# Performance work log

Measured on AMD Instinct MI355X. Metric: run time of the kernel, lower is better.

The kernel has to match this reference:

```python
import jax, jax.numpy as jnp
import numpy as np

EPS = 1e-5


def hyper_graph_conv(x, elements, W, b):
    """x: [B, C, N] vertex features; elements: [M, 8] vertex ids per hex element.
    Gather 8 vertex features per element, apply Linear(8C -> 8Co) on the
    concatenated features, then scatter-mean the 8 outputs back to vertices.
    Returns [B, Co, N]."""
    B, C, N = x.shape
    M = elements.shape[0]
    Co = W.shape[0] // 8
    g = x[:, :, elements]                      # [B, C, M, 8]
    g = jnp.transpose(g, (0, 2, 3, 1)).reshape(B, M, 8 * C)   # [B, M, 8C]
    h = jnp.einsum('bmk,ok->bmo', g, W) + b    # [B, M, 8Co]
    h = h.reshape(B, M * 8, Co)                # per-(element,corner) vertex outputs
    flat = elements.reshape(-1)                # [M*8]
    out = jnp.zeros((B, N, Co), dtype=x.dtype).at[:, flat, :].add(h)
    cnt = jnp.zeros((N,), dtype=x.dtype).at[flat].add(1.0)
    out = out / jnp.maximum(cnt, 1.0)[None, :, None]
    return jnp.transpose(out, (0, 2, 1))       # [B, Co, N]


def batch_norm(x, gamma, beta):
    # BatchNorm1d in training mode over [B, C, N]: stats over (B, N)
    mean = jnp.mean(x, axis=(0, 2), keepdims=True)
    var = jnp.mean(jnp.square(x - mean), axis=(0, 2), keepdims=True)
    xn = (x - mean) * jax.lax.rsqrt(var + EPS)
    return xn * gamma[None, :, None] + beta[None, :, None]


def setup_inputs() -> dict:
    key = jax.random.key(0)
    ks = jax.random.split(key, 8)
    B, Cin, Cout, N, M = 4, 8, 16, 100000, 98304
    return {
        'x': jax.random.normal(ks[0], (B, Cin, N), dtype=jnp.float32),
        'elements': jax.random.randint(ks[1], (M, 8), 0, N, dtype=jnp.int32),
        'W1': jax.random.normal(ks[2], (8 * Cout, 8 * Cin), dtype=jnp.float32) * (1.0 / np.sqrt(8 * Cin)),
        'b1': jnp.zeros((8 * Cout,), dtype=jnp.float32),
        'gamma1': jnp.ones((Cout,), dtype=jnp.float32),
        'beta1': jnp.zeros((Cout,), dtype=jnp.float32),
        'W2': jax.random.normal(ks[3], (8 * Cout, 8 * Cout), dtype=jnp.float32) * (1.0 / np.sqrt(8 * Cout)),
        'b2': jnp.zeros((8 * Cout,), dtype=jnp.float32),
        'gamma2': jnp.ones((Cout,), dtype=jnp.float32),
        'beta2': jnp.zeros((Cout,), dtype=jnp.float32),
        'Wskip': jax.random.normal(ks[4], (Cout, Cin), dtype=jnp.float32) * (1.0 / np.sqrt(Cin)),
        'bskip': jnp.zeros((Cout,), dtype=jnp.float32),
    }


def reference(x, elements, W1, b1, gamma1, beta1, W2, b2, gamma2, beta2, Wskip, bskip):
    out = hyper_graph_conv(x, elements, W1, b1)        # [B, Cout, N]
    out = jax.nn.relu(batch_norm(out, gamma1, beta1))
    out = hyper_graph_conv(out, elements, W2, b2)      # [B, Cout, N]
    out = batch_norm(out, gamma2, beta2)
    skip = jnp.einsum('bcn,oc->bon', x, Wskip) + bskip[None, :, None]  # Conv1d k=1
    out = jax.nn.relu(out + skip)
    return out
```

## Files before the change

### kernel.cpp

```cpp
#include <hip/hip_runtime.h>

#define NB 4
#define CIN 8
#define CO 16
#define NV 100000
#define NM 98304
#define NPOS (NM*8)
#define NBLK ((NV+255)/256)
#define VPW 14
#define REDB 1786

typedef short s16x8 __attribute__((ext_vector_type(8)));
typedef float f32x4 __attribute__((ext_vector_type(4)));
typedef unsigned short u16;
typedef unsigned int u32;

#define OFF_CNT   0
#define OFF_NEXT  400128
#define OFF_STAT  800256
#define OFF_ROWS  800640
#define OFF_BSUM  1200768
#define OFF_POS   1202432
#define OFF_XTB   4348160
#define OFF_W1B   10748160
#define OFF_W2B   10764544
#define OFF_H1    10797312
#define OFF_MBUF  23597312
#define OFF_HBUF  49197312
#define WS_NEED   149860608

static __device__ __forceinline__ u16 f2bf(float f){
  union { float f; u32 u; } v; v.f = f;
  u32 r = v.u + 0x7fffu + ((v.u >> 16) & 1u);
  return (u16)(r >> 16);
}
static __device__ __forceinline__ float bf2f_lo(u32 w){
  union { u32 u; float f; } v; v.u = w << 16; return v.f;
}
static __device__ __forceinline__ float bf2f_hi(u32 w){
  union { u32 u; float f; } v; v.u = w & 0xffff0000u; return v.f;
}
static __device__ __forceinline__ u32 pk2(float a, float b){
  return (u32)f2bf(a) | (((u32)f2bf(b)) << 16);
}

__global__ __launch_bounds__(256) void k_prep(const int* __restrict__ elem,
    const float* __restrict__ x, const float* __restrict__ W1, const float* __restrict__ W2,
    int* __restrict__ cnt, u16* __restrict__ xtb, u16* __restrict__ w1b, u16* __restrict__ w2b)
{
  __shared__ float tile[32][257];
  if (blockIdx.x < NBLK){
    int t = threadIdx.x;
    int v0 = blockIdx.x*256;
    #pragma unroll
    for (int r = 0; r < 32; r++){
      int v = v0 + t;
      tile[r][t] = (v < NV) ? x[(size_t)r*NV + v] : 0.f;
    }
    __syncthreads();
    int v = v0 + t;
    if (v < NV){
      u16 o[32] __attribute__((aligned(16)));
      #pragma unroll
      for (int r = 0; r < 32; r++) o[r] = f2bf(tile[r][t]);
      uint4* dst = (uint4*)(xtb + (size_t)v*32);
      #pragma unroll
      for (int k = 0; k < 4; k++) dst[k] = *(uint4*)(o + k*8);
    }
  } else {
    const int T1 = NPOS;
    const int T2 = T1 + 128*64;
    const int T3 = T2 + 128*128;
    int stride = (gridDim.x - NBLK)*256;
    for (int i = (blockIdx.x - NBLK)*256 + threadIdx.x; i < T3; i += stride){
      if (i < T1) { atomicAdd(cnt + elem[i], 1); }
      else if (i < T2){ int j = i - T1; w1b[j] = f2bf(W1[j]); }
      else { int j = i - T2; w2b[j] = f2bf(W2[j]); }
    }
  }
}

__global__ __launch_bounds__(256) void k_scan_a(const int* __restrict__ cnt, int* __restrict__ bsum)
{
  int v = blockIdx.x*256 + threadIdx.x;
  int x = (v < NV) ? cnt[v] : 0;
  #pragma unroll
  for (int off = 32; off > 0; off >>= 1) x += __shfl_down(x, off);
  __shared__ int ls[4];
  int wid = threadIdx.x >> 6, lane = threadIdx.x & 63;
  if (lane == 0) ls[wid] = x;
  __syncthreads();
  if (threadIdx.x == 0) bsum[blockIdx.x] = ls[0] + ls[1] + ls[2] + ls[3];
}

__global__ __launch_bounds__(256) void k_scan_c(const int* __restrict__ cnt,
    const int* __restrict__ bsum, int* __restrict__ rows)
{
  int wid = threadIdx.x >> 6, lane = threadIdx.x & 63;
  int v = blockIdx.x*256 + threadIdx.x;
  int x = (v < NV) ? cnt[v] : 0;
  int incl = x;
  #pragma unroll
  for (int off = 1; off <= 32; off <<= 1){
    int y = __shfl_up(incl, off);
    if (lane >= off) incl += y;
  }
  __shared__ int wt[4];
  __shared__ int sbase;
  if (lane == 63) wt[wid] = incl;
  if (threadIdx.x < 64){
    int s = 0;
    for (int i = threadIdx.x; i < blockIdx.x; i += 64) s += bsum[i];
    #pragma unroll
    for (int off = 32; off > 0; off >>= 1) s += __shfl_down(s, off);
    if (threadIdx.x == 0) sbase = s;
  }
  __syncthreads();
  int woff = 0;
  for (int w = 0; w < 4; w++) if (w < wid) woff += wt[w];
  if (v < NV) rows[v] = sbase + woff + incl - x;
}

__global__ __launch_bounds__(256) void k_pos(const int* __restrict__ elem,
    const int* __restrict__ rows, int* __restrict__ next, int* __restrict__ pos)
{
  int i = blockIdx.x*256 + threadIdx.x;
  if (i < NPOS){
    int v = elem[i];
    int old = atomicAdd(next + v, 1);
    pos[i] = rows[v] + old;
  }
}

__global__ __launch_bounds__(256) void k_conv1(const int* __restrict__ elem,
    const u16* __restrict__ xtb, const u16* __restrict__ w1b,
    const float* __restrict__ b1, const int* __restrict__ pos, u16* __restrict__ hbuf)
{
  const int lane = threadIdx.x & 63;
  const int col = lane & 15, kg = lane >> 4, b = lane & 3;
  s16x8 wf[8][2];
  #pragma unroll
  for (int j2 = 0; j2 < 8; j2++)
    #pragma unroll
    for (int t = 0; t < 2; t++)
      wf[j2][t] = *(const s16x8*)(w1b + (j2*16 + col)*64 + t*32 + kg*8);
  float bb[8];
  #pragma unroll
  for (int j2 = 0; j2 < 8; j2++) bb[j2] = b1[j2*16 + col];

  int wave = (int)((blockIdx.x*blockDim.x + threadIdx.x) >> 6);
  int g0 = wave, g1 = wave + 12288;
  int ma0 = g0*4 + (col >> 2), ma1 = g1*4 + (col >> 2);
  int me0 = g0*4 + kg,         me1 = g1*4 + kg;

  int e00 = elem[ma0*8 + kg], e01 = elem[ma0*8 + 4 + kg];
  int e10 = elem[ma1*8 + kg], e11 = elem[ma1*8 + 4 + kg];
  int4 p0l = *(const int4*)(pos + me0*8), p0h = *(const int4*)(pos + me0*8 + 4);
  int4 p1l = *(const int4*)(pos + me1*8), p1h = *(const int4*)(pos + me1*8 + 4);
  s16x8 a00 = *(const s16x8*)(xtb + (size_t)e00*32 + b*8);
  s16x8 a01 = *(const s16x8*)(xtb + (size_t)e01*32 + b*8);
  s16x8 a10 = *(const s16x8*)(xtb + (size_t)e10*32 + b*8);
  s16x8 a11 = *(const s16x8*)(xtb + (size_t)e11*32 + b*8);

  int pe0[8] = {p0l.x,p0l.y,p0l.z,p0l.w,p0h.x,p0h.y,p0h.z,p0h.w};
  int pe1[8] = {p1l.x,p1l.y,p1l.z,p1l.w,p1h.x,p1h.y,p1h.z,p1h.w};

  #pragma unroll
  for (int j2 = 0; j2 < 8; j2++){
    f32x4 c = {0.f,0.f,0.f,0.f};
    c = __builtin_amdgcn_mfma_f32_16x16x32_bf16(a00, wf[j2][0], c, 0, 0, 0);
    c = __builtin_amdgcn_mfma_f32_16x16x32_bf16(a01, wf[j2][1], c, 0, 0, 0);
    uint2 d; d.x = pk2(c[0]+bb[j2], c[1]+bb[j2]); d.y = pk2(c[2]+bb[j2], c[3]+bb[j2]);
    *(uint2*)(hbuf + (size_t)pe0[j2]*64 + col*4) = d;
  }
  #pragma unroll
  for (int j2 = 0; j2 < 8; j2++){
    f32x4 c = {0.f,0.f,0.f,0.f};
    c = __builtin_amdgcn_mfma_f32_16x16x32_bf16(a10, wf[j2][0], c, 0, 0, 0);
    c = __builtin_amdgcn_mfma_f32_16x16x32_bf16(a11, wf[j2][1], c, 0, 0, 0);
    uint2 d; d.x = pk2(c[0]+bb[j2], c[1]+bb[j2]); d.y = pk2(c[2]+bb[j2], c[3]+bb[j2]);
    *(uint2*)(hbuf + (size_t)pe1[j2]*64 + col*4) = d;
  }
}

__global__ __launch_bounds__(256) void k_conv2(const int* __restrict__ elem,
    const u16* __restrict__ h1, const u16* __restrict__ w2b,
    const float* __restrict__ b2, const int* __restrict__ pos, u16* __restrict__ hbuf)
{
  __shared__ u16 wl[16384];
  #pragma unroll
  for (int r = 0; r < 8; r++){
    int q = threadIdx.x + 256*r;
    int j2t = q >> 6, ln = q & 63;
    int cc = ln & 15, kk = ln >> 4;
    int j2 = j2t >> 2, tt = j2t & 3;
    *(s16x8*)(wl + (size_t)q*8) =
        *(const s16x8*)(w2b + (j2*16 + cc)*128 + tt*32 + kk*8);
  }

  const int lane = threadIdx.x & 63;
  const int col = lane & 15, kg = lane >> 4, b = lane & 3;
  const int p = kg >> 1;
  const int c0 = (kg & 1)*8;
  float bb[8];
  #pragma unroll
  for (int j2 = 0; j2 < 8; j2++) bb[j2] = b2[j2*16 + col];

  int wave = (int)((blockIdx.x*blockDim.x + threadIdx.x) >> 6);
  int g0 = wave, g1 = wave + 12288;
  int ma0 = g0*4 + (col >> 2), ma1 = g1*4 + (col >> 2);
  int me0 = g0*4 + kg,         me1 = g1*4 + kg;

  int4 e0l = *(const int4*)(elem + ma0*8), e0h = *(const int4*)(elem + ma0*8 + 4);
  int4 e1l = *(const int4*)(elem + ma1*8), e1h = *(const int4*)(elem + ma1*8 + 4);
  int4 p0l = *(const int4*)(pos + me0*8),  p0h = *(const int4*)(pos + me0*8 + 4);
  int4 p1l = *(const int4*)(pos + me1*8),  p1h = *(const int4*)(pos + me1*8 + 4);

  int v00 = p ? e0l.y : e0l.x, v01 = p ? e0l.w : e0l.z;
  int v02 = p ? e0h.y : e0h.x, v03 = p ? e0h.w : e0h.z;
  int v10 = p ? e1l.y : e1l.x, v11 = p ? e1l.w : e1l.z;
  int v12 = p ? e1h.y : e1h.x, v13 = p ? e1h.w : e1h.z;

  s16x8 af0[4], af1[4];
  af0[0] = *(const s16x8*)(h1 + (size_t)v00*64 + b*16 + c0);
  af0[1] = *(const s16x8*)(h1 + (size_t)v01*64 + b*16 + c0);
  af0[2] = *(const s16x8*)(h1 + (size_t)v02*64 + b*16 + c0);
  af0[3] = *(const s16x8*)(h1 + (size_t)v03*64 + b*16 + c0);
  af1[0] = *(const s16x8*)(h1 + (size_t)v10*64 + b*16 + c0);
  af1[1] = *(const s16x8*)(h1 + (size_t)v11*64 + b*16 + c0);
  af1[2] = *(const s16x8*)(h1 + (size_t)v12*64 + b*16 + c0);
  af1[3] = *(const s16x8*)(h1 + (size_t)v13*64 + b*16 + c0);

  int pe0[8] = {p0l.x,p0l.y,p0l.z,p0l.w,p0h.x,p0h.y,p0h.z,p0h.w};
  int pe1[8] = {p1l.x,p1l.y,p1l.z,p1l.w,p1h.x,p1h.y,p1h.z,p1h.w};

  __syncthreads();

  #pragma unroll
  for (int j2 = 0; j2 < 8; j2++){
    s16x8 w0 = *(const s16x8*)(wl + ((size_t)(j2*4 + 0)*64 + lane)*8);
    s16x8 w1 = *(const s16x8*)(wl + ((size_t)(j2*4 + 1)*64 + lane)*8);
    s16x8 w2 = *(const s16x8*)(wl + ((size_t)(j2*4 + 2)*64 + lane)*8);
    s16x8 w3 = *(const s16x8*)(wl + ((size_t)(j2*4 + 3)*64 + lane)*8);
    f32x4 c = {0.f,0.f,0.f,0.f};
    c = __builtin_amdgcn_mfma_f32_16x16x32_bf16(af0[0], w0, c, 0, 0, 0);
    c = __builtin_amdgcn_mfma_f32_16x16x32_bf16(af0[1], w1, c, 0, 0, 0);
    c = __builtin_amdgcn_mfma_f32_16x16x32_bf16(af0[2], w2, c, 0, 0, 0);
    c = __builtin_amdgcn_mfma_f32_16x16x32_bf16(af0[3], w3, c, 0, 0, 0);
    uint2 d; d.x = pk2(c[0]+bb[j2], c[1]+bb[j2]); d.y = pk2(c[2]+bb[j2], c[3]+bb[j2]);
    *(uint2*)(hbuf + (size_t)pe0[j2]*64 + col*4) = d;
  }
  #pragma unroll
  for (int j2 = 0; j2 < 8; j2++){
    s16x8 w0 = *(const s16x8*)(wl + ((size_t)(j2*4 + 0)*64 + lane)*8);
    s16x8 w1 = *(const s16x8*)(wl + ((size_t)(j2*4 + 1)*64 + lane)*8);
    s16x8 w2 = *(const s16x8*)(wl + ((size_t)(j2*4 + 2)*64 + lane)*8);
    s16x8 w3 = *(const s16x8*)(wl + ((size_t)(j2*4 + 3)*64 + lane)*8);
    f32x4 c = {0.f,0.f,0.f,0.f};
    c = __builtin_amdgcn_mfma_f32_16x16x32_bf16(af1[0], w0, c, 0, 0, 0);
    c = __builtin_amdgcn_mfma_f32_16x16x32_bf16(af1[1], w1, c, 0, 0, 0);
    c = __builtin_amdgcn_mfma_f32_16x16x32_bf16(af1[2], w2, c, 0, 0, 0);
    c = __builtin_amdgcn_mfma_f32_16x16x32_bf16(af1[3], w3, c, 0, 0, 0);
    uint2 d; d.x = pk2(c[0]+bb[j2], c[1]+bb[j2]); d.y = pk2(c[2]+bb[j2], c[3]+bb[j2]);
    *(uint2*)(hbuf + (size_t)pe1[j2]*64 + col*4) = d;
  }
}

__global__ __launch_bounds__(256) void k_reduce(const u16* __restrict__ hbuf,
    const int* __restrict__ rows, u16* __restrict__ mbuf, float* __restrict__ stat)
{
  int lane = threadIdx.x & 63, wid = threadIdx.x >> 6;
  int half = lane >> 5;
  int hl   = lane & 31;
  int k8   = lane & 7;
  int rg   = (lane >> 3) & 3;
  int w = (blockIdx.x*blockDim.x + threadIdx.x) >> 6;
  int v0 = w * VPW;

  int vv = v0 + lane;
  int rr = 0;
  if (lane < VPW + 1) rr = (vv < NV) ? rows[vv] : NPOS;

  int rs[7], ce[7];
  #pragma unroll
  for (int j = 0; j < 7; j++){
    rs[j] = __shfl(rr, 2*j + half);
    ce[j] = __shfl(rr, 2*j + half + 1) - rs[j];
  }

  uint4 d0[7], d1[7];
  #pragma unroll
  for (int j = 0; j < 7; j++){
    uint4 z = {0u,0u,0u,0u};
    d0[j] = z; d1[j] = z;
    const u16* base = hbuf + (size_t)rs[j]*64 + hl*8;
    if (rg     < ce[j]) d0[j] = *(const uint4*)(base);
    if (4 + rg < ce[j]) d1[j] = *(const uint4*)(base + 4*64);
  }

  float st_s0 = 0.f, st_q0 = 0.f, st_s1 = 0.f, st_q1 = 0.f;

  #pragma unroll
  for (int j = 0; j < 7; j++){
    float a0,a1,a2,a3,a4,a5,a6,a7;
    {
      uint4 dA = d0[j], dB = d1[j];
      a0 = bf2f_lo(dA.x)+bf2f_lo(dB.x); a1 = bf2f_hi(dA.x)+bf2f_hi(dB.x);
      a2 = bf2f_lo(dA.y)+bf2f_lo(dB.y); a3 = bf2f_hi(dA.y)+bf2f_hi(dB.y);
      a4 = bf2f_lo(dA.z)+bf2f_lo(dB.z); a5 = bf2f_hi(dA.z)+bf2f_hi(dB.z);
      a6 = bf2f_lo(dA.w)+bf2f_lo(dB.w); a7 = bf2f_hi(dA.w)+bf2f_hi(dB.w);
    }
    for (int p = 8; p < ce[j]; p += 4){
      uint4 d = {0u,0u,0u,0u};
      if (p + rg < ce[j]) d = *(const uint4*)(hbuf + (size_t)(rs[j]+p)*64 + hl*8);
      a0 += bf2f_lo(d.x); a1 += bf2f_hi(d.x); a2 += bf2f_lo(d.y); a3 += bf2f_hi(d.y);
      a4 += bf2f_lo(d.z); a5 += bf2f_hi(d.z); a6 += bf2f_lo(d.w); a7 += bf2f_hi(d.w);
    }
    #pragma unroll
    for (int off = 8; off <= 16; off <<= 1){
      a0 += __shfl_xor(a0, off); a1 += __shfl_xor(a1, off);
      a2 += __shfl_xor(a2, off); a3 += __shfl_xor(a3, off);
      a4 += __shfl_xor(a4, off); a5 += __shfl_xor(a5, off);
      a6 += __shfl_xor(a6, off); a7 += __shfl_xor(a7, off);
    }
    int v = v0 + 2*j + half;
    if (hl < 8 && v < NV){
      float inv = 1.0f / fmaxf((float)ce[j], 1.0f);
      float c0b[4] = {a0*inv, a1*inv, a2*inv, a3*inv};
      float c1b[4] = {a4*inv, a5*inv, a6*inv, a7*inv};
      #pragma unroll
      for (int q = 0; q < 4; q++){
        *(u32*)(mbuf + (size_t)v*64 + q*16 + 2*k8) = pk2(c0b[q], c1b[q]);
        st_s0 += c0b[q]; st_q0 += c0b[q]*c0b[q];
        st_s1 += c1b[q]; st_q1 += c1b[q]*c1b[q];
      }
    }
  }

  st_s0 += __shfl_xor(st_s0, 32); st_q0 += __shfl_xor(st_q0, 32);
  st_s1 += __shfl_xor(st_s1, 32); st_q1 += __shfl_xor(st_q1, 32);
  __shared__ float ls[4][16], lq[4][16];
  if (lane < 8){
    ls[wid][2*k8] = st_s0; ls[wid][2*k8+1] = st_s1;
    lq[wid][2*k8] = st_q0; lq[wid][2*k8+1] = st_q1;
  }
  __syncthreads();
  if (threadIdx.x < 32){
    int c2 = threadIdx.x & 15, which = threadIdx.x >> 4;
    float tot = 0.f;
    #pragma unroll
    for (int w2 = 0; w2 < 4; w2++) tot += which ? lq[w2][c2] : ls[w2][c2];
    unsafeAtomicAdd(stat + which*16 + c2, tot);
  }
}

__global__ __launch_bounds__(256) void k_apply1(const u16* __restrict__ mbuf,
    const float* __restrict__ stat, const float* __restrict__ gamma,
    const float* __restrict__ beta, u16* __restrict__ h1)
{
  __shared__ float sc[16], sh[16];
  if (threadIdx.x < 16){
    int co = threadIdx.x;
    const float invn = 1.0f / (float)(NB*NV);
    float m = stat[co]*invn;
    float var = stat[16+co]*invn - m*m;
    float s = gamma[co]*rsqrtf(var + 1e-5f);
    sc[co] = s; sh[co] = beta[co] - m*s;
  }
  __syncthreads();
  int idx = blockIdx.x*256 + threadIdx.x;
  int v = idx >> 2, b = idx & 3;
  if (v >= NV) return;
  const uint4* src = (const uint4*)(mbuf + (size_t)v*64 + b*16);
  uint4 m0 = src[0], m1 = src[1];
  u32 mw[8] = {m0.x,m0.y,m0.z,m0.w,m1.x,m1.y,m1.z,m1.w};
  u16 o[16] __attribute__((aligned(16)));
  #pragma unroll
  for (int k = 0; k < 8; k++){
    int c0 = 2*k, c1 = 2*k + 1;
    float va = bf2f_lo(mw[k])*sc[c0] + sh[c0];
    float vb = bf2f_hi(mw[k])*sc[c1] + sh[c1];
    o[c0] = f2bf(fmaxf(va, 0.f));
    o[c1] = f2bf(fmaxf(vb, 0.f));
  }
  uint4* dst = (uint4*)(h1 + (size_t)v*64 + b*16);
  dst[0] = *(uint4*)(o);
  dst[1] = *(uint4*)(o + 8);
}

__global__ __launch_bounds__(256) void k_final(const u16* __restrict__ mbuf,
    const float* __restrict__ stat, const float* __restrict__ gamma,
    const float* __restrict__ beta, const float* __restrict__ x,
    const float* __restrict__ wsk, const float* __restrict__ bsk, float* __restrict__ out)
{
  __shared__ float sc[16], sh[16];
  if (threadIdx.x < 16){
    int co = threadIdx.x;
    const float invn = 1.0f / (float)(NB*NV);
    float m = stat[co]*invn;
    float var = stat[16+co]*invn - m*m;
    float s = gamma[co]*rsqrtf(var + 1e-5f);
    sc[co] = s; sh[co] = beta[co] - m*s + bsk[co];
  }
  __syncthreads();
  int n = blockIdx.x*blockDim.x + threadIdx.x;
  int b = blockIdx.y;
  if (n >= NV) return;
  float xv[8];
  #pragma unroll
  for (int c = 0; c < 8; c++) xv[c] = x[((size_t)b*8 + c)*NV + n];
  const uint4* src = (const uint4*)(mbuf + (size_t)n*64 + b*16);
  uint4 m0 = src[0], m1 = src[1];
  u32 mw[8] = {m0.x,m0.y,m0.z,m0.w,m1.x,m1.y,m1.z,m1.w};
  #pragma unroll
  for (int k = 0; k < 8; k++){
    #pragma unroll
    for (int h = 0; h < 2; h++){
      int co = 2*k + h;
      float val = (h ? bf2f_hi(mw[k]) : bf2f_lo(mw[k]))*sc[co] + sh[co];
      #pragma unroll
      for (int c = 0; c < 8; c++) val += wsk[co*8+c]*xv[c];
      out[((size_t)b*16 + co)*NV + n] = fmaxf(val, 0.f);
    }
  }
}

extern "C" void kernel_launch(void* const* d_in, const int* in_sizes, int n_in,
                              void* d_out, int out_size, void* d_ws, size_t ws_size,
                              hipStream_t stream) {
  const float* x    = (const float*)d_in[0];
  const int*   elem = (const int*)  d_in[1];
  const float* W1   = (const float*)d_in[2];
  const float* b1   = (const float*)d_in[3];
  const float* g1   = (const float*)d_in[4];
  const float* be1  = (const float*)d_in[5];
  const float* W2   = (const float*)d_in[6];
  const float* b2   = (const float*)d_in[7];
  const float* g2   = (const float*)d_in[8];
  const float* be2  = (const float*)d_in[9];
  const float* Wsk  = (const float*)d_in[10];
  const float* bsk  = (const float*)d_in[11];
  float* out = (float*)d_out;

  if (ws_size < (size_t)WS_NEED) return;

  char* ws = (char*)d_ws;
  int*   cnt  = (int*)  (ws + OFF_CNT);
  int*   next = (int*)  (ws + OFF_NEXT);
  float* stat = (float*)(ws + OFF_STAT);
  int*   rows = (int*)  (ws + OFF_ROWS);
  int*   bsum = (int*)  (ws + OFF_BSUM);
  int*   pos  = (int*)  (ws + OFF_POS);
  u16*   xtb  = (u16*)  (ws + OFF_XTB);
  u16*   w1b  = (u16*)  (ws + OFF_W1B);
  u16*   w2b  = (u16*)  (ws + OFF_W2B);
  u16*   h1   = (u16*)  (ws + OFF_H1);
  u16*   mbuf = (u16*)  (ws + OFF_MBUF);
  u16*   hbuf = (u16*)  (ws + OFF_HBUF);

  hipMemsetAsync(ws, 0, OFF_STAT + 384, stream);

  k_prep<<<NBLK + 1024, 256, 0, stream>>>(elem, x, W1, W2, cnt, xtb, w1b, w2b);
  k_scan_a<<<NBLK, 256, 0, stream>>>(cnt, bsum);
  k_scan_c<<<NBLK, 256, 0, stream>>>(cnt, bsum, rows);
  k_pos<<<NPOS/256, 256, 0, stream>>>(elem, rows, next, pos);

  k_conv1<<<3072, 256, 0, stream>>>(elem, xtb, w1b, b1, pos, hbuf);
  k_reduce<<<REDB, 256, 0, stream>>>(hbuf, rows, mbuf, stat);
  k_apply1<<<(NV*4 + 255)/256, 256, 0, stream>>>(mbuf, stat, g1, be1, h1);

  k_conv2<<<3072, 256, 0, stream>>>(elem, h1, w2b, b2, pos, hbuf);
  k_reduce<<<REDB, 256, 0, stream>>>(hbuf, rows, mbuf, stat + 32);
  k_final<<<dim3((NV+255)/256, NB), 256, 0, stream>>>(mbuf, stat + 32, g2, be2, x, Wsk, bsk, out);
}
```

Baseline: 259.6 us.

## Replace global-atomic vertex counting and slot assignment with LDS-binned histograms

Vertex degree counting and CSR slot assignment move from global atomics to 64 blocks. Each block owns a range of 1563 vertices, scans the entire element list, and applies LDS atomics only to ids in its range. This removes contended global atomics and the 800KB memset of cnt/next, but every block now reads the full 3MB element array (64x redundant reads) with only 64 workgroups active. The x transpose is split into its own kernel.

```diff
diff --git a/kernel.cpp b/kernel.cpp
--- a/kernel.cpp
+++ b/kernel.cpp
@@ -9,6 +9,8 @@
 #define NBLK ((NV+255)/256)
 #define VPW 14
 #define REDB 1786
+#define CB 64
+#define BINS 1563
 
 typedef short s16x8 __attribute__((ext_vector_type(8)));
 typedef float f32x4 __attribute__((ext_vector_type(4)));
@@ -44,40 +46,57 @@
   return (u32)f2bf(a) | (((u32)f2bf(b)) << 16);
 }
 
-__global__ __launch_bounds__(256) void k_prep(const int* __restrict__ elem,
-    const float* __restrict__ x, const float* __restrict__ W1, const float* __restrict__ W2,
-    int* __restrict__ cnt, u16* __restrict__ xtb, u16* __restrict__ w1b, u16* __restrict__ w2b)
+__global__ __launch_bounds__(256) void k_xt(const float* __restrict__ x, u16* __restrict__ xtb)
 {
   __shared__ float tile[32][257];
-  if (blockIdx.x < NBLK){
-    int t = threadIdx.x;
-    int v0 = blockIdx.x*256;
-    #pragma unroll
-    for (int r = 0; r < 32; r++){
-      int v = v0 + t;
-      tile[r][t] = (v < NV) ? x[(size_t)r*NV + v] : 0.f;
+  int t = threadIdx.x;
+  int v0 = blockIdx.x*256;
+  #pragma unroll
+  for (int r = 0; r < 32; r++){
+    int v = v0 + t;
+    tile[r][t] = (v < NV) ? x[(size_t)r*NV + v] : 0.f;
+  }
+  __syncthreads();
+  int v = v0 + t;
+  if (v < NV){
+    u16 o[32] __attribute__((aligned(16)));
+    #pragma unroll
+    for (int r = 0; r < 32; r++) o[r] = f2bf(tile[r][t]);
+    uint4* dst = (uint4*)(xtb + (size_t)v*32);
+    #pragma unroll
+    for (int k = 0; k < 4; k++) dst[k] = *(uint4*)(o + k*8);
+  }
+}
+
+__global__ __launch_bounds__(1024) void k_count(const int* __restrict__ elem,
+    const float* __restrict__ W1, const float* __restrict__ W2,
+    int* __restrict__ cnt, u16* __restrict__ w1b, u16* __restrict__ w2b)
+{
+  if (blockIdx.x >= CB){
+    const int T1 = 128*64, T2 = T1 + 128*128;
+    for (int i = (blockIdx.x - CB)*1024 + threadIdx.x; i < T2; i += 2048){
+      if (i < T1) w1b[i] = f2bf(W1[i]);
+      else { int j = i - T1; w2b[j] = f2bf(W2[j]); }
     }
-    __syncthreads();
-    int v = v0 + t;
-    if (v < NV){
-      u16 o[32] __attribute__((aligned(16)));
-      #pragma unroll
-      for (int r = 0; r < 32; r++) o[r] = f2bf(tile[r][t]);
-      uint4* dst = (uint4*)(xtb + (size_t)v*32);
-      #pragma unroll
-      for (int k = 0; k < 4; k++) dst[k] = *(uint4*)(o + k*8);
-    }
-  } else {
-    const int T1 = NPOS;
-    const int T2 = T1 + 128*64;
-    const int T3 = T2 + 128*128;
-    int stride = (gridDim.x - NBLK)*256;
-    for (int i = (blockIdx.x - NBLK)*256 + threadIdx.x; i < T3; i += stride){
-      if (i < T1) { atomicAdd(cnt + elem[i], 1); }
-      else if (i < T2){ int j = i - T1; w1b[j] = f2bf(W1[j]); }
-      else { int j = i - T2; w2b[j] = f2bf(W2[j]); }
-    }
-  }
+    return;
+  }
+  __shared__ int lh[BINS];
+  int base = blockIdx.x * BINS;
+  for (int j = threadIdx.x; j < BINS; j += 1024) lh[j] = 0;
+  __syncthreads();
+  const int4* e4 = (const int4*)elem;
+  for (int j = threadIdx.x; j < NPOS/4; j += 1024){
+    int4 q = e4[j];
+    u32 u0 = (u32)(q.x - base), u1 = (u32)(q.y - base);
+    u32 u2 = (u32)(q.z - base), u3 = (u32)(q.w - base);
+    if (u0 < (u32)BINS) atomicAdd(&lh[u0], 1);
+    if (u1 < (u32)BINS) atomicAdd(&lh[u1], 1);
+    if (u2 < (u32)BINS) atomicAdd(&lh[u2], 1);
+    if (u3 < (u32)BINS) atomicAdd(&lh[u3], 1);
+  }
+  __syncthreads();
+  for (int j = threadIdx.x; j < BINS; j += 1024)
+    if (base + j < NV) cnt[base + j] = lh[j];
 }
 
 __global__ __launch_bounds__(256) void k_scan_a(const int* __restrict__ cnt, int* __restrict__ bsum)
@@ -121,14 +140,27 @@
   if (v < NV) rows[v] = sbase + woff + incl - x;
 }
 
-__global__ __launch_bounds__(256) void k_pos(const int* __restrict__ elem,
-    const int* __restrict__ rows, int* __restrict__ next, int* __restrict__ pos)
-{
-  int i = blockIdx.x*256 + threadIdx.x;
-  if (i < NPOS){
-    int v = elem[i];
-    int old = atomicAdd(next + v, 1);
-    pos[i] = rows[v] + old;
+__global__ __launch_bounds__(1024) void k_assign(const int* __restrict__ elem,
+    const int* __restrict__ rows, int* __restrict__ pos)
+{
+  __shared__ int lnext[BINS];
+  __shared__ int lrows[BINS];
+  int base = blockIdx.x * BINS;
+  for (int j = threadIdx.x; j < BINS; j += 1024){
+    lnext[j] = 0;
+    lrows[j] = (base + j < NV) ? rows[base + j] : 0;
+  }
+  __syncthreads();
+  const int4* e4 = (const int4*)elem;
+  for (int j = threadIdx.x; j < NPOS/4; j += 1024){
+    int4 q = e4[j];
+    int i0 = 4*j;
+    u32 u0 = (u32)(q.x - base), u1 = (u32)(q.y - base);
+    u32 u2 = (u32)(q.z - base), u3 = (u32)(q.w - base);
+    if (u0 < (u32)BINS){ int old = atomicAdd(&lnext[u0], 1); pos[i0    ] = lrows[u0] + old; }
+    if (u1 < (u32)BINS){ int old = atomicAdd(&lnext[u1], 1); pos[i0 + 1] = lrows[u1] + old; }
+    if (u2 < (u32)BINS){ int old = atomicAdd(&lnext[u2], 1); pos[i0 + 2] = lrows[u2] + old; }
+    if (u3 < (u32)BINS){ int old = atomicAdd(&lnext[u3], 1); pos[i0 + 3] = lrows[u3] + old; }
   }
 }
 
@@ -446,7 +478,6 @@
 
   char* ws = (char*)d_ws;
   int*   cnt  = (int*)  (ws + OFF_CNT);
-  int*   next = (int*)  (ws + OFF_NEXT);
   float* stat = (float*)(ws + OFF_STAT);
   int*   rows = (int*)  (ws + OFF_ROWS);
   int*   bsum = (int*)  (ws + OFF_BSUM);
@@ -458,12 +489,13 @@
   u16*   mbuf = (u16*)  (ws + OFF_MBUF);
   u16*   hbuf = (u16*)  (ws + OFF_HBUF);
 
-  hipMemsetAsync(ws, 0, OFF_STAT + 384, stream);
-
-  k_prep<<<NBLK + 1024, 256, 0, stream>>>(elem, x, W1, W2, cnt, xtb, w1b, w2b);
+  hipMemsetAsync(ws + OFF_STAT, 0, 384, stream);
+
+  k_xt<<<NBLK, 256, 0, stream>>>(x, xtb);
+  k_count<<<CB + 2, 1024, 0, stream>>>(elem, W1, W2, cnt, w1b, w2b);
   k_scan_a<<<NBLK, 256, 0, stream>>>(cnt, bsum);
   k_scan_c<<<NBLK, 256, 0, stream>>>(cnt, bsum, rows);
-  k_pos<<<NPOS/256, 256, 0, stream>>>(elem, rows, next, pos);
+  k_assign<<<CB, 1024, 0, stream>>>(elem, rows, pos);
 
   k_conv1<<<3072, 256, 0, stream>>>(elem, xtb, w1b, b1, pos, hbuf);
   k_reduce<<<REDB, 256, 0, stream>>>(hbuf, rows, mbuf, stat);
```

After: 354.2 us. 1.36x slower.

## Replace double-atomic CSR build with replicated counters and single-pass slot assignment

Applied to the files above, without the earlier changes.

The per-vertex counting pass and the separate position-assignment pass, both of which used global atomics over all element corners, are merged into one atomic pass. That pass records each corner's slot from the atomicAdd return value, and spreads contention across 8 replicated counter arrays chosen by block index. The scan kernels sum the replicas and write a per-replica base offset, so a final non-atomic pass can compute positions with vectorized int4 loads. The x transpose is split into its own kernel. The cost is an extra 3.2 MB memset, replica reads in the scans, and a larger workspace requirement.

```diff
diff --git a/kernel.cpp b/kernel.cpp
--- a/kernel.cpp
+++ b/kernel.cpp
@@ -4,6 +4,7 @@
 #define CIN 8
 #define CO 16
 #define NV 100000
+#define NVP 100096
 #define NM 98304
 #define NPOS (NM*8)
 #define NBLK ((NV+255)/256)
@@ -15,8 +16,6 @@
 typedef unsigned short u16;
 typedef unsigned int u32;
 
-#define OFF_CNT   0
-#define OFF_NEXT  400128
 #define OFF_STAT  800256
 #define OFF_ROWS  800640
 #define OFF_BSUM  1200768
@@ -27,7 +26,9 @@
 #define OFF_H1    10797312
 #define OFF_MBUF  23597312
 #define OFF_HBUF  49197312
-#define WS_NEED   149860608
+#define OFF_CNTR  149860608
+#define OFF_BASER (OFF_CNTR + 8*NVP*4)
+#define WS_NEED   (OFF_BASER + 8*NVP*4)
 
 static __device__ __forceinline__ u16 f2bf(float f){
   union { float f; u32 u; } v; v.f = f;
@@ -44,46 +45,60 @@
   return (u32)f2bf(a) | (((u32)f2bf(b)) << 16);
 }
 
-__global__ __launch_bounds__(256) void k_prep(const int* __restrict__ elem,
-    const float* __restrict__ x, const float* __restrict__ W1, const float* __restrict__ W2,
-    int* __restrict__ cnt, u16* __restrict__ xtb, u16* __restrict__ w1b, u16* __restrict__ w2b)
+__global__ __launch_bounds__(256) void k_xt(const float* __restrict__ x, u16* __restrict__ xtb)
 {
   __shared__ float tile[32][257];
-  if (blockIdx.x < NBLK){
-    int t = threadIdx.x;
-    int v0 = blockIdx.x*256;
-    #pragma unroll
-    for (int r = 0; r < 32; r++){
-      int v = v0 + t;
-      tile[r][t] = (v < NV) ? x[(size_t)r*NV + v] : 0.f;
+  int t = threadIdx.x;
+  int v0 = blockIdx.x*256;
+  #pragma unroll
+  for (int r = 0; r < 32; r++){
+    int v = v0 + t;
+    tile[r][t] = (v < NV) ? x[(size_t)r*NV + v] : 0.f;
+  }
+  __syncthreads();
+  int v = v0 + t;
+  if (v < NV){
+    u16 o[32] __attribute__((aligned(16)));
+    #pragma unroll
+    for (int r = 0; r < 32; r++) o[r] = f2bf(tile[r][t]);
+    uint4* dst = (uint4*)(xtb + (size_t)v*32);
+    #pragma unroll
+    for (int k = 0; k < 4; k++) dst[k] = *(uint4*)(o + k*8);
+  }
+}
+
+__global__ __launch_bounds__(256) void k_slot(const int* __restrict__ elem,
+    const float* __restrict__ W1, const float* __restrict__ W2,
+    int* __restrict__ cntR, int* __restrict__ slot,
+    u16* __restrict__ w1b, u16* __restrict__ w2b)
+{
+  int b = blockIdx.x;
+  if (b >= 1024){
+    const int T1 = 128*64, T2 = T1 + 128*128;
+    for (int i = (b - 1024)*256 + threadIdx.x; i < T2; i += 8*256){
+      if (i < T1) w1b[i] = f2bf(W1[i]);
+      else { int j = i - T1; w2b[j] = f2bf(W2[j]); }
     }
-    __syncthreads();
-    int v = v0 + t;
-    if (v < NV){
-      u16 o[32] __attribute__((aligned(16)));
-      #pragma unroll
-      for (int r = 0; r < 32; r++) o[r] = f2bf(tile[r][t]);
-      uint4* dst = (uint4*)(xtb + (size_t)v*32);
-      #pragma unroll
-      for (int k = 0; k < 4; k++) dst[k] = *(uint4*)(o + k*8);
-    }
-  } else {
-    const int T1 = NPOS;
-    const int T2 = T1 + 128*64;
-    const int T3 = T2 + 128*128;
-    int stride = (gridDim.x - NBLK)*256;
-    for (int i = (blockIdx.x - NBLK)*256 + threadIdx.x; i < T3; i += stride){
-      if (i < T1) { atomicAdd(cnt + elem[i], 1); }
-      else if (i < T2){ int j = i - T1; w1b[j] = f2bf(W1[j]); }
-      else { int j = i - T2; w2b[j] = f2bf(W2[j]); }
-    }
-  }
-}
-
-__global__ __launch_bounds__(256) void k_scan_a(const int* __restrict__ cnt, int* __restrict__ bsum)
+    return;
+  }
+  int* myc = cntR + (b & 7)*NVP;
+  int i0 = b*768 + threadIdx.x;
+  #pragma unroll
+  for (int k = 0; k < 3; k++){
+    int i = i0 + k*256;
+    int v = elem[i];
+    slot[i] = atomicAdd(myc + v, 1);
+  }
+}
+
+__global__ __launch_bounds__(256) void k_scan_a(const int* __restrict__ cntR, int* __restrict__ bsum)
 {
   int v = blockIdx.x*256 + threadIdx.x;
-  int x = (v < NV) ? cnt[v] : 0;
+  int x = 0;
+  if (v < NV){
+    #pragma unroll
+    for (int r = 0; r < 8; r++) x += cntR[r*NVP + v];
+  }
   #pragma unroll
   for (int off = 32; off > 0; off >>= 1) x += __shfl_down(x, off);
   __shared__ int ls[4];
@@ -93,12 +108,17 @@
   if (threadIdx.x == 0) bsum[blockIdx.x] = ls[0] + ls[1] + ls[2] + ls[3];
 }
 
-__global__ __launch_bounds__(256) void k_scan_c(const int* __restrict__ cnt,
-    const int* __restrict__ bsum, int* __restrict__ rows)
+__global__ __launch_bounds__(256) void k_scan_c(const int* __restrict__ cntR,
+    const int* __restrict__ bsum, int* __restrict__ rows, int* __restrict__ baseR)
 {
   int wid = threadIdx.x >> 6, lane = threadIdx.x & 63;
   int v = blockIdx.x*256 + threadIdx.x;
-  int x = (v < NV) ? cnt[v] : 0;
+  int cr[8];
+  #pragma unroll
+  for (int r = 0; r < 8; r++) cr[r] = (v < NV) ? cntR[r*NVP + v] : 0;
+  int pre[8]; int x = 0;
+  #pragma unroll
+  for (int r = 0; r < 8; r++){ pre[r] = x; x += cr[r]; }
   int incl = x;
   #pragma unroll
   for (int off = 1; off <= 32; off <<= 1){
@@ -118,18 +138,28 @@
   __syncthreads();
   int woff = 0;
   for (int w = 0; w < 4; w++) if (w < wid) woff += wt[w];
-  if (v < NV) rows[v] = sbase + woff + incl - x;
-}
-
-__global__ __launch_bounds__(256) void k_pos(const int* __restrict__ elem,
-    const int* __restrict__ rows, int* __restrict__ next, int* __restrict__ pos)
-{
-  int i = blockIdx.x*256 + threadIdx.x;
-  if (i < NPOS){
-    int v = elem[i];
-    int old = atomicAdd(next + v, 1);
-    pos[i] = rows[v] + old;
-  }
+  if (v < NV){
+    int row0 = sbase + woff + incl - x;
+    rows[v] = row0;
+    #pragma unroll
+    for (int r = 0; r < 8; r++) baseR[r*NVP + v] = row0 + pre[r];
+  }
+}
+
+__global__ __launch_bounds__(256) void k_pos2(const int* __restrict__ elem,
+    const int* __restrict__ baseR, int* __restrict__ pos)
+{
+  int i4 = blockIdx.x*256 + threadIdx.x;
+  int4 e = ((const int4*)elem)[i4];
+  int4 s = ((const int4*)pos)[i4];
+  int r = ((i4*4)/768) & 7;
+  const int* br = baseR + r*NVP;
+  int4 p;
+  p.x = br[e.x] + s.x;
+  p.y = br[e.y] + s.y;
+  p.z = br[e.z] + s.z;
+  p.w = br[e.w] + s.w;
+  ((int4*)pos)[i4] = p;
 }
 
 __global__ __launch_bounds__(256) void k_conv1(const int* __restrict__ elem,
@@ -445,25 +475,27 @@
   if (ws_size < (size_t)WS_NEED) return;
 
   char* ws = (char*)d_ws;
-  int*   cnt  = (int*)  (ws + OFF_CNT);
-  int*   next = (int*)  (ws + OFF_NEXT);
-  float* stat = (float*)(ws + OFF_STAT);
-  int*   rows = (int*)  (ws + OFF_ROWS);
-  int*   bsum = (int*)  (ws + OFF_BSUM);
-  int*   pos  = (int*)  (ws + OFF_POS);
-  u16*   xtb  = (u16*)  (ws + OFF_XTB);
-  u16*   w1b  = (u16*)  (ws + OFF_W1B);
-  u16*   w2b  = (u16*)  (ws + OFF_W2B);
-  u16*   h1   = (u16*)  (ws + OFF_H1);
-  u16*   mbuf = (u16*)  (ws + OFF_MBUF);
-  u16*   hbuf = (u16*)  (ws + OFF_HBUF);
-
-  hipMemsetAsync(ws, 0, OFF_STAT + 384, stream);
-
-  k_prep<<<NBLK + 1024, 256, 0, stream>>>(elem, x, W1, W2, cnt, xtb, w1b, w2b);
-  k_scan_a<<<NBLK, 256, 0, stream>>>(cnt, bsum);
-  k_scan_c<<<NBLK, 256, 0, stream>>>(cnt, bsum, rows);
-  k_pos<<<NPOS/256, 256, 0, stream>>>(elem, rows, next, pos);
+  float* stat  = (float*)(ws + OFF_STAT);
+  int*   rows  = (int*)  (ws + OFF_ROWS);
+  int*   bsum  = (int*)  (ws + OFF_BSUM);
+  int*   pos   = (int*)  (ws + OFF_POS);
+  u16*   xtb   = (u16*)  (ws + OFF_XTB);
+  u16*   w1b   = (u16*)  (ws + OFF_W1B);
+  u16*   w2b   = (u16*)  (ws + OFF_W2B);
+  u16*   h1    = (u16*)  (ws + OFF_H1);
+  u16*   mbuf  = (u16*)  (ws + OFF_MBUF);
+  u16*   hbuf  = (u16*)  (ws + OFF_HBUF);
+  int*   cntR  = (int*)  (ws + OFF_CNTR);
+  int*   baseR = (int*)  (ws + OFF_BASER);
+
+  hipMemsetAsync(ws + OFF_CNTR, 0, 8*NVP*4, stream);
+  hipMemsetAsync(ws + OFF_STAT, 0, 384, stream);
+
+  k_xt<<<NBLK, 256, 0, stream>>>(x, xtb);
+  k_slot<<<1032, 256, 0, stream>>>(elem, W1, W2, cntR, pos, w1b, w2b);
+  k_scan_a<<<NBLK, 256, 0, stream>>>(cntR, bsum);
+  k_scan_c<<<NBLK, 256, 0, stream>>>(cntR, bsum, rows, baseR);
+  k_pos2<<<768, 256, 0, stream>>>(elem, baseR, pos);
 
   k_conv1<<<3072, 256, 0, stream>>>(elem, xtb, w1b, b1, pos, hbuf);
   k_reduce<<<REDB, 256, 0, stream>>>(hbuf, rows, mbuf, stat);
```

Measured after the change: 239.1 us. 1.09x faster.
